# Optimization experiments

Measured on AMD Instinct MI355X. Metric: run time of the kernel, lower is better.

The kernel has to match this reference:

```python
import jax, jax.numpy as jnp
import numpy as np

N, E = 100000, 1600000
DIN, DH, DOUT = 256, 128, 32


def _glorot(key, fan_in, fan_out):
    lim = np.sqrt(6.0 / (fan_in + fan_out)).astype(np.float32)
    return jax.random.uniform(key, (fan_in, fan_out), jnp.float32, -lim, lim)


def setup_inputs() -> dict:
    key = jax.random.key(0)
    k0, k1, k2, k3 = jax.random.split(key, 4)
    x = jax.random.normal(k0, (N, DIN), dtype=jnp.float32)
    edge_index = jax.random.randint(k1, (2, E), 0, N, dtype=jnp.int64)
    return {
        "x": x,
        "edge_index": edge_index,
        "W1": _glorot(k2, DIN, DH),
        "b1": jnp.zeros((DH,), jnp.float32),
        "W2": _glorot(k3, DH, DOUT),
        "b2": jnp.zeros((DOUT,), jnp.float32),
    }


def _gcn_conv(h_in, W, b, src, dst, deg_norm_src, deg_norm_dst, n):
    # PyG GCNConv: linear transform, then sym-normalized scatter-add, then bias.
    h = h_in @ W                                   # [N, F_out]
    msg = h[src] * (deg_norm_src * deg_norm_dst)[:, None]  # [E+N, F_out]
    agg = jax.ops.segment_sum(msg, dst, num_segments=n)    # [N, F_out]
    return agg + b


def reference(x, edge_index, W1, b1, W2, b2):
    n = x.shape[0]
    loops = jnp.arange(n, dtype=edge_index.dtype)  # self-loops (GCNConv default)
    src = jnp.concatenate([edge_index[0], loops])
    dst = jnp.concatenate([edge_index[1], loops])
    deg = jax.ops.segment_sum(jnp.ones(src.shape[0], x.dtype), dst, num_segments=n)
    dis = jnp.where(deg > 0, jax.lax.rsqrt(deg), 0.0)  # deg^{-1/2}
    ns, nd = dis[src], dis[dst]
    h = jax.nn.relu(_gcn_conv(x, W1, b1, src, dst, ns, nd, n))
    out = _gcn_conv(h, W2, b2, src, dst, ns, nd, n)
    return jax.nn.log_softmax(out, axis=1)
```

## Files before the change

### kernel.cpp

```cpp
#include <hip/hip_runtime.h>
#include <hip/hip_bf16.h>
#include <cstdint>

#define DIN 256
#define DH 128
#define DOUT 32
#define CE 4096
#define BSH 9
#define MAXW 12288

typedef short s16x8 __attribute__((ext_vector_type(8)));
typedef float f32x4 __attribute__((ext_vector_type(4)));

__device__ inline ushort f2bf(float f) {
    uint u = __float_as_uint(f);
    u += 0x7fff + ((u >> 16) & 1);
    return (ushort)(u >> 16);
}
__device__ inline ushort cvtbf(float f) {
    __hip_bfloat16 b = __float2bfloat16(f);
    return __builtin_bit_cast(ushort, b);
}
__device__ inline float bf_lo(uint u) { return __uint_as_float(u << 16); }
__device__ inline float bf_hi(uint u) { return __uint_as_float(u & 0xffff0000u); }
__device__ inline uint packbf(float a, float b) {
    return (uint)cvtbf(a) | ((uint)cvtbf(b) << 16);
}
__device__ inline float ub0(uint v) { return (float)(v & 0xFFu); }
__device__ inline float ub1(uint v) { return (float)((v >> 8) & 0xFFu); }
__device__ inline float ub2(uint v) { return (float)((v >> 16) & 0xFFu); }
__device__ inline float ub3(uint v) { return (float)(v >> 24); }


__global__ __launch_bounds__(256) void k_prep(const float* __restrict__ W1,
                                              ushort* __restrict__ w1tg) {
    int o = blockIdx.x * 1024 + threadIdx.x * 4;
    int c = o >> 8;
    int k = o & 255;
    ushort4 v;
    v.x = f2bf(W1[(size_t)(k + 0) * DH + c]);
    v.y = f2bf(W1[(size_t)(k + 1) * DH + c]);
    v.z = f2bf(W1[(size_t)(k + 2) * DH + c]);
    v.w = f2bf(W1[(size_t)(k + 3) * DH + c]);
    *(ushort4*)(w1tg + o) = v;
}


__global__ __launch_bounds__(256) void k_part(
    const int* __restrict__ src, const int* __restrict__ dst,
    uint* __restrict__ pairs, int* __restrict__ tbl, int* __restrict__ gctr,
    int e, int nbuck) {
    __shared__ int cnt[256];
    __shared__ int boffs[256];
    __shared__ int sh[256];
    __shared__ uint ps[CE];
    int tid = threadIdx.x;
    if (blockIdx.x == 0 && tid == 0) *gctr = 0;
    long blkbase = (long)blockIdx.x * CE;
    int ecnt = min(CE, (int)(e - blkbase));

    cnt[tid] = 0;
    __syncthreads();

    int dreg[CE / 256];
    #pragma unroll
    for (int k = 0; k < CE / 256; ++k) {
        int i = k * 256 + tid;
        int d = -1;
        if (i < ecnt) {
            d = dst[blkbase + i];
            atomicAdd(&cnt[d >> BSH], 1);
        }
        dreg[k] = d;
    }
    __syncthreads();
    sh[tid] = cnt[tid];
    __syncthreads();
    for (int off = 1; off < 256; off <<= 1) {
        int x = (tid >= off) ? sh[tid - off] : 0;
        __syncthreads();
        if (tid >= off) sh[tid] += x;
        __syncthreads();
    }
    boffs[tid] = (tid == 0) ? 0 : sh[tid - 1];
    cnt[tid] = 0;
    __syncthreads();
    #pragma unroll
    for (int k = 0; k < CE / 256; ++k) {
        int i = k * 256 + tid;
        if (i < ecnt) {
            int d = dreg[k];
            int b = d >> BSH;
            int slot = boffs[b] + atomicAdd(&cnt[b], 1);
            ps[slot] = ((uint)(d & 511) << 17) | (uint)src[blkbase + i];
        }
    }
    __syncthreads();
    for (int i = tid; i < ecnt; i += 256)
        pairs[blkbase + i] = ps[i];
    if (tid < nbuck) tbl[blockIdx.x * (nbuck + 1) + tid] = boffs[tid];
    if (tid == 0)    tbl[blockIdx.x * (nbuck + 1) + nbuck] = ecnt;
}


__global__ __launch_bounds__(256) void k_build(
    const uint* __restrict__ pairs, const int* __restrict__ tbl,
    int* __restrict__ deg, int* __restrict__ offs, float* __restrict__ dis,
    int* __restrict__ adj, int* __restrict__ gctr,
    int nblk1, int nbuck, int n) {
    __shared__ int indeg[512];
    __shared__ int excl[512];
    __shared__ int sh[256];
    __shared__ int adjS[MAXW];
    __shared__ int baseSh, totSh;
    int tid = threadIdx.x;
    int b = blockIdx.x;
    int nodebase = b << BSH;

    indeg[tid] = 0;
    indeg[tid + 256] = 0;
    __syncthreads();

    for (int run = tid; run < nblk1; run += 256) {
        const int* trow = tbl + run * (nbuck + 1);
        int s0 = trow[b], s1 = trow[b + 1];
        long base = (long)run * CE;
        for (int k = s0; k < s1; ++k) {
            uint pp = pairs[base + k];
            atomicAdd(&indeg[pp >> 17], 1);
        }
    }
    __syncthreads();

    int a0 = indeg[tid * 2];
    int a1 = indeg[tid * 2 + 1];
    sh[tid] = a0 + a1;
    __syncthreads();
    for (int off = 1; off < 256; off <<= 1) {
        int x = (tid >= off) ? sh[tid - off] : 0;
        __syncthreads();
        if (tid >= off) sh[tid] += x;
        __syncthreads();
    }
    int e0 = (tid == 0) ? 0 : sh[tid - 1];
    excl[tid * 2] = e0;
    excl[tid * 2 + 1] = e0 + a0;
    if (tid == 255) {
        totSh = sh[255];
        baseSh = atomicAdd(gctr, sh[255]);
    }
    __syncthreads();
    int base = baseSh;
    int L = totSh;

    int i0 = nodebase + tid * 2;
    if (i0 < n) {
        deg[i0] = a0 + 1;
        offs[i0] = base + excl[tid * 2];
        dis[i0] = rsqrtf((float)(a0 + 1));
    }
    if (i0 + 1 < n) {
        deg[i0 + 1] = a1 + 1;
        offs[i0 + 1] = base + excl[tid * 2 + 1];
        dis[i0 + 1] = rsqrtf((float)(a1 + 1));
    }
    indeg[tid] = 0;
    indeg[tid + 256] = 0;
    __syncthreads();

    if (L <= MAXW) {
        for (int run = tid; run < nblk1; run += 256) {
            const int* trow = tbl + run * (nbuck + 1);
            int s0 = trow[b], s1 = trow[b + 1];
            long pb = (long)run * CE;
            for (int k = s0; k < s1; ++k) {
                uint pp = pairs[pb + k];
                int local = pp >> 17;
                int pos = excl[local] + atomicAdd(&indeg[local], 1);
                adjS[pos] = (int)(pp & 0x1FFFFu);
            }
        }
        __syncthreads();
        for (int i = tid; i < L; i += 256) adj[base + i] = adjS[i];
    } else {
        for (int run = tid; run < nblk1; run += 256) {
            const int* trow = tbl + run * (nbuck + 1);
            int s0 = trow[b], s1 = trow[b + 1];
            long pb = (long)run * CE;
            for (int k = s0; k < s1; ++k) {
                uint pp = pairs[pb + k];
                int local = pp >> 17;
                int pos = base + excl[local] + atomicAdd(&indeg[local], 1);
                adj[pos] = (int)(pp & 0x1FFFFu);
            }
        }
    }
}


__global__ __launch_bounds__(256) void k_gemm1(
    const float* __restrict__ x, const ushort* __restrict__ w1tg,
    const float* __restrict__ dis, uchar* __restrict__ hs8,
    float* __restrict__ scl, int n) {
    __shared__ union {
        ushort w1t[128][136];
        uchar  cs8[128][144];
    } u;
    __shared__ ushort xs[128][72];

    int tid = threadIdx.x;
    int row0 = blockIdx.x * 128;
    int lane = tid & 63;
    int w = tid >> 6;
    int wr0 = w * 32;
    int l15 = lane & 15;
    int koff = (lane >> 4) * 8;

    f32x4 acc[2][8];
    #pragma unroll
    for (int i = 0; i < 2; ++i)
        #pragma unroll
        for (int j = 0; j < 8; ++j)
            acc[i][j] = (f32x4){0.f, 0.f, 0.f, 0.f};

    for (int kh = 0; kh < 2; ++kh) {
        {
            int c = tid >> 1;
            int seg = (tid & 1) * 64;
            const uint4* gsrc = (const uint4*)(w1tg + (size_t)c * 256 + kh * 128 + seg);
            uint4* ldst = (uint4*)&u.w1t[c][seg];
            #pragma unroll
            for (int q = 0; q < 8; ++q) ldst[q] = gsrc[q];
        }
        for (int kc2 = 0; kc2 < 2; ++kc2) {
            {
                int r = tid >> 1;
                int half = (tid & 1) * 32;
                int rr = row0 + r; if (rr >= n) rr = n - 1;
                const float4* xr = (const float4*)(x + (size_t)rr * DIN + kh * 128 + kc2 * 64 + half);
                float4 v[8];
                #pragma unroll
                for (int q = 0; q < 8; ++q) v[q] = xr[q];
                #pragma unroll
                for (int q = 0; q < 8; ++q) {
                    ushort4 o;
                    o.x = cvtbf(v[q].x); o.y = cvtbf(v[q].y);
                    o.z = cvtbf(v[q].z); o.w = cvtbf(v[q].w);
                    *(ushort4*)&xs[r][half + q * 4] = o;
                }
            }
            __syncthreads();
            #pragma unroll
            for (int kk = 0; kk < 64; kk += 32) {
                s16x8 a0 = *(const s16x8*)&xs[wr0 + l15][kk + koff];
                s16x8 a1 = *(const s16x8*)&xs[wr0 + 16 + l15][kk + koff];
                int kl = kc2 * 64 + kk + koff;
                #pragma unroll
                for (int ct = 0; ct < 8; ++ct) {
                    s16x8 b = *(const s16x8*)&u.w1t[ct * 16 + l15][kl];
                    acc[0][ct] = __builtin_amdgcn_mfma_f32_16x16x32_bf16(a0, b, acc[0][ct], 0, 0, 0);
                    acc[1][ct] = __builtin_amdgcn_mfma_f32_16x16x32_bf16(a1, b, acc[1][ct], 0, 0, 0);
                }
            }
            __syncthreads();
        }
    }

    float dv[2][4];
    #pragma unroll
    for (int rt = 0; rt < 2; ++rt)
        #pragma unroll
        for (int r = 0; r < 4; ++r) {
            int rg = row0 + wr0 + rt * 16 + (lane >> 4) * 4 + r;
            if (rg >= n) rg = n - 1;
            dv[rt][r] = dis[rg];
        }
    #pragma unroll
    for (int rt = 0; rt < 2; ++rt) {
        #pragma unroll
        for (int r = 0; r < 4; ++r) {
            int lrow = wr0 + rt * 16 + (lane >> 4) * 4 + r;
            float vals[8];
            float mx = 0.f;
            #pragma unroll
            for (int ct = 0; ct < 8; ++ct) {
                vals[ct] = acc[rt][ct][r] * dv[rt][r];
                mx = fmaxf(mx, fabsf(vals[ct]));
            }
            mx = fmaxf(mx, __shfl_xor(mx, 1));
            mx = fmaxf(mx, __shfl_xor(mx, 2));
            mx = fmaxf(mx, __shfl_xor(mx, 4));
            mx = fmaxf(mx, __shfl_xor(mx, 8));
            float s = mx * (1.f / 127.f);
            float inv = (mx > 0.f) ? 127.f / mx : 0.f;
            #pragma unroll
            for (int ct = 0; ct < 8; ++ct)
                u.cs8[lrow][ct * 16 + l15] = (uchar)(__float2int_rn(vals[ct] * inv) + 128);
            if (l15 == 0 && row0 + lrow < n) scl[row0 + lrow] = s;
        }
    }
    __syncthreads();
    {
        int r = tid >> 1;
        int half = (tid & 1) * 64;
        if (row0 + r < n) {
            uint4* dstp = (uint4*)(hs8 + (size_t)(row0 + r) * 128 + half);
            const uint4* sp = (const uint4*)&u.cs8[r][half];
            #pragma unroll
            for (int q = 0; q < 4; ++q) dstp[q] = sp[q];
        }
    }
}


__global__ __launch_bounds__(256) void k_agg1(
    const uchar* __restrict__ hs8, const float* __restrict__ scl,
    const float* __restrict__ dis, const int* __restrict__ offs,
    const int* __restrict__ deg, const int* __restrict__ adj,
    const float* __restrict__ b1, ushort* __restrict__ h1, int n) {
    int node = blockIdx.x * 4 + (threadIdx.x >> 6);
    if (node >= n) return;
    int lane = threadIdx.x & 63;
    int r = lane >> 4;
    int j = lane & 15;

    const uint2* hq = (const uint2*)hs8;
    int off = offs[node];
    int nsrc = deg[node];

    float a8[8] = {0.f, 0.f, 0.f, 0.f, 0.f, 0.f, 0.f, 0.f};
    float ss = 0.f;
    int i = r;
    #define ACC8(v, c)                                      \
        a8[0] += ub0((v).x) * (c); a8[1] += ub1((v).x) * (c); \
        a8[2] += ub2((v).x) * (c); a8[3] += ub3((v).x) * (c); \
        a8[4] += ub0((v).y) * (c); a8[5] += ub1((v).y) * (c); \
        a8[6] += ub2((v).y) * (c); a8[7] += ub3((v).y) * (c); \
        ss += (c);
    for (; i + 12 < nsrc; i += 16) {
        int s0 = (i == 0) ? node : adj[off + i - 1];
        int s1 = adj[off + i + 3];
        int s2 = adj[off + i + 7];
        int s3 = adj[off + i + 11];
        float c0 = scl[s0], c1 = scl[s1], c2 = scl[s2], c3 = scl[s3];
        uint2 v0 = hq[(size_t)s0 * 16 + j];
        uint2 v1 = hq[(size_t)s1 * 16 + j];
        uint2 v2 = hq[(size_t)s2 * 16 + j];
        uint2 v3 = hq[(size_t)s3 * 16 + j];
        ACC8(v0, c0) ACC8(v1, c1) ACC8(v2, c2) ACC8(v3, c3)
    }
    for (; i + 4 < nsrc; i += 8) {
        int s0 = (i == 0) ? node : adj[off + i - 1];
        int s1 = adj[off + i + 3];
        float c0 = scl[s0], c1 = scl[s1];
        uint2 v0 = hq[(size_t)s0 * 16 + j];
        uint2 v1 = hq[(size_t)s1 * 16 + j];
        ACC8(v0, c0) ACC8(v1, c1)
    }
    if (i < nsrc) {
        int s0 = (i == 0) ? node : adj[off + i - 1];
        float c0 = scl[s0];
        uint2 v0 = hq[(size_t)s0 * 16 + j];
        ACC8(v0, c0)
    }
    #undef ACC8
    #pragma unroll
    for (int q = 0; q < 8; ++q) {
        a8[q] += __shfl_xor(a8[q], 16);
        a8[q] += __shfl_xor(a8[q], 32);
    }
    ss += __shfl_xor(ss, 16);
    ss += __shfl_xor(ss, 32);
    float corr = 128.f * ss;
    #pragma unroll
    for (int q = 0; q < 8; ++q) a8[q] -= corr;

    float dv = dis[node];
    float4 ba = ((const float4*)b1)[j * 2];
    float4 bb = ((const float4*)b1)[j * 2 + 1];
    if (r == 0) {
        uint4 ov;
        ov.x = packbf(fmaxf(a8[0] * dv + ba.x, 0.f), fmaxf(a8[1] * dv + ba.y, 0.f));
        ov.y = packbf(fmaxf(a8[2] * dv + ba.z, 0.f), fmaxf(a8[3] * dv + ba.w, 0.f));
        ov.z = packbf(fmaxf(a8[4] * dv + bb.x, 0.f), fmaxf(a8[5] * dv + bb.y, 0.f));
        ov.w = packbf(fmaxf(a8[6] * dv + bb.z, 0.f), fmaxf(a8[7] * dv + bb.w, 0.f));
        ((uint4*)h1)[(size_t)node * 16 + j] = ov;
    }
}


__global__ __launch_bounds__(256) void k_gemm2(
    const ushort* __restrict__ h1, const float* __restrict__ W2,
    const float* __restrict__ dis, uchar* __restrict__ h2q,
    float* __restrict__ scl2, int n) {
    int t = blockIdx.x * blockDim.x + threadIdx.x;
    int row = t >> 3;
    int cg = t & 7;
    if (row >= n) return;
    const uint2* hr = (const uint2*)(h1 + (size_t)row * DH);
    const float4* w4 = (const float4*)W2;
    float4 acc = make_float4(0.f, 0.f, 0.f, 0.f);
    #pragma unroll 8
    for (int k4 = 0; k4 < DH / 4; ++k4) {
        uint2 au = hr[k4];
        float a0 = bf_lo(au.x), a1 = bf_hi(au.x), a2 = bf_lo(au.y), a3 = bf_hi(au.y);
        float4 w0 = w4[(k4 * 4 + 0) * 8 + cg];
        float4 w1 = w4[(k4 * 4 + 1) * 8 + cg];
        float4 w2 = w4[(k4 * 4 + 2) * 8 + cg];
        float4 w3 = w4[(k4 * 4 + 3) * 8 + cg];
        acc.x += a0 * w0.x + a1 * w1.x + a2 * w2.x + a3 * w3.x;
        acc.y += a0 * w0.y + a1 * w1.y + a2 * w2.y + a3 * w3.y;
        acc.z += a0 * w0.z + a1 * w1.z + a2 * w2.z + a3 * w3.z;
        acc.w += a0 * w0.w + a1 * w1.w + a2 * w2.w + a3 * w3.w;
    }
    float dv = dis[row];
    float vals[4] = {acc.x * dv, acc.y * dv, acc.z * dv, acc.w * dv};
    float mx = fmaxf(fmaxf(fabsf(vals[0]), fabsf(vals[1])),
                     fmaxf(fabsf(vals[2]), fabsf(vals[3])));
    mx = fmaxf(mx, __shfl_xor(mx, 1));
    mx = fmaxf(mx, __shfl_xor(mx, 2));
    mx = fmaxf(mx, __shfl_xor(mx, 4));
    float s = mx * (1.f / 127.f);
    float inv = (mx > 0.f) ? 127.f / mx : 0.f;
    uint q0 = (uint)(__float2int_rn(vals[0] * inv) + 128);
    uint q1 = (uint)(__float2int_rn(vals[1] * inv) + 128);
    uint q2 = (uint)(__float2int_rn(vals[2] * inv) + 128);
    uint q3 = (uint)(__float2int_rn(vals[3] * inv) + 128);
    ((uint*)h2q)[(size_t)row * 8 + cg] = q0 | (q1 << 8) | (q2 << 16) | (q3 << 24);
    if (cg == 0) scl2[row] = s;
}


__global__ __launch_bounds__(256) void k_agg2_lsm(
    const uchar* __restrict__ h2q, const float* __restrict__ scl2,
    const float* __restrict__ dis, const int* __restrict__ offs,
    const int* __restrict__ deg, const int* __restrict__ adj,
    const float* __restrict__ b2, float* __restrict__ out, int n) {
    int node = blockIdx.x * 8 + (threadIdx.x >> 5);
    if (node >= n) return;
    int t32 = threadIdx.x & 31;
    int rr = t32 >> 2;
    int j = t32 & 3;

    const uint2* hq = (const uint2*)h2q;
    int off = offs[node];
    int nsrc = deg[node];

    float a8[8] = {0.f, 0.f, 0.f, 0.f, 0.f, 0.f, 0.f, 0.f};
    float ss = 0.f;
    int i = rr;
    #define ACC8(v, c)                                      \
        a8[0] += ub0((v).x) * (c); a8[1] += ub1((v).x) * (c); \
        a8[2] += ub2((v).x) * (c); a8[3] += ub3((v).x) * (c); \
        a8[4] += ub0((v).y) * (c); a8[5] += ub1((v).y) * (c); \
        a8[6] += ub2((v).y) * (c); a8[7] += ub3((v).y) * (c); \
        ss += (c);
    for (; i + 8 < nsrc; i += 16) {
        int s0 = (i == 0) ? node : adj[off + i - 1];
        int s1 = adj[off + i + 7];
        float c0 = scl2[s0], c1 = scl2[s1];
        uint2 v0 = hq[(size_t)s0 * 4 + j];
        uint2 v1 = hq[(size_t)s1 * 4 + j];
        ACC8(v0, c0) ACC8(v1, c1)
    }
    if (i < nsrc) {
        int s0 = (i == 0) ? node : adj[off + i - 1];
        float c0 = scl2[s0];
        uint2 v0 = hq[(size_t)s0 * 4 + j];
        ACC8(v0, c0)
    }
    #undef ACC8
    #pragma unroll
    for (int q = 0; q < 8; ++q) {
        a8[q] += __shfl_xor(a8[q], 4);
        a8[q] += __shfl_xor(a8[q], 8);
        a8[q] += __shfl_xor(a8[q], 16);
    }
    ss += __shfl_xor(ss, 4);
    ss += __shfl_xor(ss, 8);
    ss += __shfl_xor(ss, 16);
    float corr = 128.f * ss;
    #pragma unroll
    for (int q = 0; q < 8; ++q) a8[q] -= corr;

    float dv = dis[node];
    float4 ba = ((const float4*)b2)[j * 2];
    float4 bb = ((const float4*)b2)[j * 2 + 1];
    float v[8];
    v[0] = a8[0] * dv + ba.x; v[1] = a8[1] * dv + ba.y;
    v[2] = a8[2] * dv + ba.z; v[3] = a8[3] * dv + ba.w;
    v[4] = a8[4] * dv + bb.x; v[5] = a8[5] * dv + bb.y;
    v[6] = a8[6] * dv + bb.z; v[7] = a8[7] * dv + bb.w;
    float m = v[0];
    #pragma unroll
    for (int q = 1; q < 8; ++q) m = fmaxf(m, v[q]);
    m = fmaxf(m, __shfl_xor(m, 1));
    m = fmaxf(m, __shfl_xor(m, 2));
    float s = 0.f;
    #pragma unroll
    for (int q = 0; q < 8; ++q) s += __expf(v[q] - m);
    s += __shfl_xor(s, 1);
    s += __shfl_xor(s, 2);
    float ls = m + __logf(s);
    if (rr == 0) {
        float4 o0 = make_float4(v[0] - ls, v[1] - ls, v[2] - ls, v[3] - ls);
        float4 o1 = make_float4(v[4] - ls, v[5] - ls, v[6] - ls, v[7] - ls);
        float* op = out + (size_t)node * DOUT + j * 8;
        *(float4*)op = o0;
        *(float4*)(op + 4) = o1;
    }
}

extern "C" void kernel_launch(void* const* d_in, const int* in_sizes, int n_in,
                              void* d_out, int out_size, void* d_ws, size_t ws_size,
                              hipStream_t stream) {
    const float* x  = (const float*)d_in[0];
    const int*   ei = (const int*)d_in[1];
    const float* W1 = (const float*)d_in[2];
    const float* b1 = (const float*)d_in[3];
    const float* W2 = (const float*)d_in[4];
    const float* b2 = (const float*)d_in[5];
    int n = in_sizes[0] / DIN;
    int e = in_sizes[1] / 2;
    const int* src = ei;
    const int* dst = ei + e;
    float* out = (float*)d_out;

    int nblk1 = (e + CE - 1) / CE;
    int nbuck = (n + 511) >> BSH;

    char* p = (char*)d_ws;
    uint*   pairs  = (uint*)p;    p += (size_t)e * 4;
    int*    tbl    = (int*)p;     p += (size_t)nblk1 * (nbuck + 1) * 4;
    int*    deg    = (int*)p;     p += (size_t)n * 4;
    int*    offs   = (int*)p;     p += (size_t)n * 4;
    int*    gctr   = (int*)p;     p += 1024;
    float*  dis    = (float*)p;   p += (size_t)n * 4;
    int*    adj    = (int*)p;     p += (size_t)e * 4;
    ushort* w1tg   = (ushort*)p;  p += (size_t)DIN * DH * 2;
    uchar*  hs8    = (uchar*)p;   p += (size_t)n * DH;
    float*  scl    = (float*)p;   p += (size_t)n * 4;
    ushort* h1     = (ushort*)p;  p += (size_t)n * DH * 2;
    uchar*  h2q    = (uchar*)p;   p += (size_t)n * DOUT;
    float*  scl2   = (float*)p;

    k_prep<<<32, 256, 0, stream>>>(W1, w1tg);
    k_part<<<nblk1, 256, 0, stream>>>(src, dst, pairs, tbl, gctr, e, nbuck);
    k_build<<<nbuck, 256, 0, stream>>>(pairs, tbl, deg, offs, dis, adj, gctr,
                                       nblk1, nbuck, n);

    k_gemm1<<<(n + 127) / 128, 256, 0, stream>>>(x, w1tg, dis, hs8, scl, n);
    k_agg1<<<(n + 3) / 4, 256, 0, stream>>>(hs8, scl, dis, offs, deg, adj, b1, h1, n);
    k_gemm2<<<(n * 8 + 255) / 256, 256, 0, stream>>>(h1, W2, dis, h2q, scl2, n);
    k_agg2_lsm<<<(n + 7) / 8, 256, 0, stream>>>(h2q, scl2, dis, offs, deg, adj, b2, out, n);
}
```

Baseline: 240.7 us.

## Co-schedule GEMM1 with CSR build and fold W1 prep into partition kernel

The W1 transpose/convert blocks are merged into the edge partition kernel as extra blocks. GEMM1 and the CSR build now run as different block ranges of one launch, so the compute-bound GEMM can overlap the atomic-heavy graph build. To remove GEMM1's dependency on dis, the per-row quantization now runs on the unscaled product, and a small k_fix kernel afterwards multiplies scl by dis. This is valid because dis is a positive per-row factor. It drops launches and serialization but adds one pass over scl, and shared memory per block grows to the max of both roles.

```diff
diff --git a/kernel.cpp b/kernel.cpp
--- a/kernel.cpp
+++ b/kernel.cpp
@@ -32,29 +32,30 @@
 __device__ inline float ub3(uint v) { return (float)(v >> 24); }
 
 
-__global__ __launch_bounds__(256) void k_prep(const float* __restrict__ W1,
-                                              ushort* __restrict__ w1tg) {
-    int o = blockIdx.x * 1024 + threadIdx.x * 4;
-    int c = o >> 8;
-    int k = o & 255;
-    ushort4 v;
-    v.x = f2bf(W1[(size_t)(k + 0) * DH + c]);
-    v.y = f2bf(W1[(size_t)(k + 1) * DH + c]);
-    v.z = f2bf(W1[(size_t)(k + 2) * DH + c]);
-    v.w = f2bf(W1[(size_t)(k + 3) * DH + c]);
-    *(ushort4*)(w1tg + o) = v;
-}
-
-
-__global__ __launch_bounds__(256) void k_part(
+__global__ __launch_bounds__(256) void k_pre(
     const int* __restrict__ src, const int* __restrict__ dst,
     uint* __restrict__ pairs, int* __restrict__ tbl, int* __restrict__ gctr,
-    int e, int nbuck) {
+    const float* __restrict__ W1, ushort* __restrict__ w1tg,
+    int e, int nbuck, int nblk1) {
     __shared__ int cnt[256];
     __shared__ int boffs[256];
     __shared__ int sh[256];
     __shared__ uint ps[CE];
     int tid = threadIdx.x;
+
+    if (blockIdx.x >= nblk1) {
+        int o = (blockIdx.x - nblk1) * 1024 + tid * 4;
+        int c = o >> 8;
+        int k = o & 255;
+        ushort4 v;
+        v.x = f2bf(W1[(size_t)(k + 0) * DH + c]);
+        v.y = f2bf(W1[(size_t)(k + 1) * DH + c]);
+        v.z = f2bf(W1[(size_t)(k + 2) * DH + c]);
+        v.w = f2bf(W1[(size_t)(k + 3) * DH + c]);
+        *(ushort4*)(w1tg + o) = v;
+        return;
+    }
+
     if (blockIdx.x == 0 && tid == 0) *gctr = 0;
     long blkbase = (long)blockIdx.x * CE;
     int ecnt = min(CE, (int)(e - blkbase));
@@ -103,18 +104,123 @@
 }
 
 
-__global__ __launch_bounds__(256) void k_build(
+__global__ __launch_bounds__(256) void k_bg(
+    const float* __restrict__ x, const ushort* __restrict__ w1tg,
+    uchar* __restrict__ hs8, float* __restrict__ scl,
     const uint* __restrict__ pairs, const int* __restrict__ tbl,
     int* __restrict__ deg, int* __restrict__ offs, float* __restrict__ dis,
     int* __restrict__ adj, int* __restrict__ gctr,
-    int nblk1, int nbuck, int n) {
-    __shared__ int indeg[512];
-    __shared__ int excl[512];
-    __shared__ int sh[256];
-    __shared__ int adjS[MAXW];
-    __shared__ int baseSh, totSh;
+    int nblk1, int nbuck, int n, int ngemm) {
+    __shared__ __align__(16) char smem[54288];
     int tid = threadIdx.x;
-    int b = blockIdx.x;
+
+    if (blockIdx.x < ngemm) {
+        ushort (*w1t)[136] = (ushort(*)[136])smem;
+        uchar  (*cs8)[144] = (uchar(*)[144])smem;
+        ushort (*xs)[72]   = (ushort(*)[72])(smem + 34816);
+
+        int row0 = blockIdx.x * 128;
+        int lane = tid & 63;
+        int w = tid >> 6;
+        int wr0 = w * 32;
+        int l15 = lane & 15;
+        int koff = (lane >> 4) * 8;
+
+        f32x4 acc[2][8];
+        #pragma unroll
+        for (int i = 0; i < 2; ++i)
+            #pragma unroll
+            for (int j = 0; j < 8; ++j)
+                acc[i][j] = (f32x4){0.f, 0.f, 0.f, 0.f};
+
+        for (int kh = 0; kh < 2; ++kh) {
+            {
+                int c = tid >> 1;
+                int seg = (tid & 1) * 64;
+                const uint4* gsrc = (const uint4*)(w1tg + (size_t)c * 256 + kh * 128 + seg);
+                uint4* ldst = (uint4*)&w1t[c][seg];
+                #pragma unroll
+                for (int q = 0; q < 8; ++q) ldst[q] = gsrc[q];
+            }
+            for (int kc2 = 0; kc2 < 2; ++kc2) {
+                {
+                    int r = tid >> 1;
+                    int half = (tid & 1) * 32;
+                    int rr = row0 + r; if (rr >= n) rr = n - 1;
+                    const float4* xr = (const float4*)(x + (size_t)rr * DIN + kh * 128 + kc2 * 64 + half);
+                    float4 v[8];
+                    #pragma unroll
+                    for (int q = 0; q < 8; ++q) v[q] = xr[q];
+                    #pragma unroll
+                    for (int q = 0; q < 8; ++q) {
+                        ushort4 o;
+                        o.x = cvtbf(v[q].x); o.y = cvtbf(v[q].y);
+                        o.z = cvtbf(v[q].z); o.w = cvtbf(v[q].w);
+                        *(ushort4*)&xs[r][half + q * 4] = o;
+                    }
+                }
+                __syncthreads();
+                #pragma unroll
+                for (int kk = 0; kk < 64; kk += 32) {
+                    s16x8 a0 = *(const s16x8*)&xs[wr0 + l15][kk + koff];
+                    s16x8 a1 = *(const s16x8*)&xs[wr0 + 16 + l15][kk + koff];
+                    int kl = kc2 * 64 + kk + koff;
+                    #pragma unroll
+                    for (int ct = 0; ct < 8; ++ct) {
+                        s16x8 b = *(const s16x8*)&w1t[ct * 16 + l15][kl];
+                        acc[0][ct] = __builtin_amdgcn_mfma_f32_16x16x32_bf16(a0, b, acc[0][ct], 0, 0, 0);
+                        acc[1][ct] = __builtin_amdgcn_mfma_f32_16x16x32_bf16(a1, b, acc[1][ct], 0, 0, 0);
+                    }
+                }
+                __syncthreads();
+            }
+        }
+
+        #pragma unroll
+        for (int rt = 0; rt < 2; ++rt) {
+            #pragma unroll
+            for (int r = 0; r < 4; ++r) {
+                int lrow = wr0 + rt * 16 + (lane >> 4) * 4 + r;
+                float vals[8];
+                float mx = 0.f;
+                #pragma unroll
+                for (int ct = 0; ct < 8; ++ct) {
+                    vals[ct] = acc[rt][ct][r];
+                    mx = fmaxf(mx, fabsf(vals[ct]));
+                }
+                mx = fmaxf(mx, __shfl_xor(mx, 1));
+                mx = fmaxf(mx, __shfl_xor(mx, 2));
+                mx = fmaxf(mx, __shfl_xor(mx, 4));
+                mx = fmaxf(mx, __shfl_xor(mx, 8));
+                float s = mx * (1.f / 127.f);
+                float inv = (mx > 0.f) ? 127.f / mx : 0.f;
+                #pragma unroll
+                for (int ct = 0; ct < 8; ++ct)
+                    cs8[lrow][ct * 16 + l15] = (uchar)(__float2int_rn(vals[ct] * inv) + 128);
+                if (l15 == 0 && row0 + lrow < n) scl[row0 + lrow] = s;
+            }
+        }
+        __syncthreads();
+        {
+            int r = tid >> 1;
+            int half = (tid & 1) * 64;
+            if (row0 + r < n) {
+                uint4* dstp = (uint4*)(hs8 + (size_t)(row0 + r) * 128 + half);
+                const uint4* sp = (const uint4*)&cs8[r][half];
+                #pragma unroll
+                for (int q = 0; q < 4; ++q) dstp[q] = sp[q];
+            }
+        }
+        return;
+    }
+
+    int* adjS  = (int*)smem;
+    int* indeg = (int*)(smem + 49152);
+    int* excl  = (int*)(smem + 51200);
+    int* shb   = (int*)(smem + 53248);
+    int* bt    = (int*)(smem + 54272);
+
+    int b = blockIdx.x - ngemm;
     int nodebase = b << BSH;
 
     indeg[tid] = 0;
@@ -134,24 +240,24 @@
 
     int a0 = indeg[tid * 2];
     int a1 = indeg[tid * 2 + 1];
-    sh[tid] = a0 + a1;
+    shb[tid] = a0 + a1;
     __syncthreads();
     for (int off = 1; off < 256; off <<= 1) {
-        int x = (tid >= off) ? sh[tid - off] : 0;
+        int xv = (tid >= off) ? shb[tid - off] : 0;
         __syncthreads();
-        if (tid >= off) sh[tid] += x;
+        if (tid >= off) shb[tid] += xv;
         __syncthreads();
     }
-    int e0 = (tid == 0) ? 0 : sh[tid - 1];
+    int e0 = (tid == 0) ? 0 : shb[tid - 1];
     excl[tid * 2] = e0;
     excl[tid * 2 + 1] = e0 + a0;
     if (tid == 255) {
-        totSh = sh[255];
-        baseSh = atomicAdd(gctr, sh[255]);
-    }
-    __syncthreads();
-    int base = baseSh;
-    int L = totSh;
+        bt[1] = shb[255];
+        bt[0] = atomicAdd(gctr, shb[255]);
+    }
+    __syncthreads();
+    int base = bt[0];
+    int L = bt[1];
 
     int i0 = nodebase + tid * 2;
     if (i0 < n) {
@@ -198,118 +304,9 @@
 }
 
 
-__global__ __launch_bounds__(256) void k_gemm1(
-    const float* __restrict__ x, const ushort* __restrict__ w1tg,
-    const float* __restrict__ dis, uchar* __restrict__ hs8,
-    float* __restrict__ scl, int n) {
-    __shared__ union {
-        ushort w1t[128][136];
-        uchar  cs8[128][144];
-    } u;
-    __shared__ ushort xs[128][72];
-
-    int tid = threadIdx.x;
-    int row0 = blockIdx.x * 128;
-    int lane = tid & 63;
-    int w = tid >> 6;
-    int wr0 = w * 32;
-    int l15 = lane & 15;
-    int koff = (lane >> 4) * 8;
-
-    f32x4 acc[2][8];
-    #pragma unroll
-    for (int i = 0; i < 2; ++i)
-        #pragma unroll
-        for (int j = 0; j < 8; ++j)
-            acc[i][j] = (f32x4){0.f, 0.f, 0.f, 0.f};
-
-    for (int kh = 0; kh < 2; ++kh) {
-        {
-            int c = tid >> 1;
-            int seg = (tid & 1) * 64;
-            const uint4* gsrc = (const uint4*)(w1tg + (size_t)c * 256 + kh * 128 + seg);
-            uint4* ldst = (uint4*)&u.w1t[c][seg];
-            #pragma unroll
-            for (int q = 0; q < 8; ++q) ldst[q] = gsrc[q];
-        }
-        for (int kc2 = 0; kc2 < 2; ++kc2) {
-            {
-                int r = tid >> 1;
-                int half = (tid & 1) * 32;
-                int rr = row0 + r; if (rr >= n) rr = n - 1;
-                const float4* xr = (const float4*)(x + (size_t)rr * DIN + kh * 128 + kc2 * 64 + half);
-                float4 v[8];
-                #pragma unroll
-                for (int q = 0; q < 8; ++q) v[q] = xr[q];
-                #pragma unroll
-                for (int q = 0; q < 8; ++q) {
-                    ushort4 o;
-                    o.x = cvtbf(v[q].x); o.y = cvtbf(v[q].y);
-                    o.z = cvtbf(v[q].z); o.w = cvtbf(v[q].w);
-                    *(ushort4*)&xs[r][half + q * 4] = o;
-                }
-            }
-            __syncthreads();
-            #pragma unroll
-            for (int kk = 0; kk < 64; kk += 32) {
-                s16x8 a0 = *(const s16x8*)&xs[wr0 + l15][kk + koff];
-                s16x8 a1 = *(const s16x8*)&xs[wr0 + 16 + l15][kk + koff];
-                int kl = kc2 * 64 + kk + koff;
-                #pragma unroll
-                for (int ct = 0; ct < 8; ++ct) {
-                    s16x8 b = *(const s16x8*)&u.w1t[ct * 16 + l15][kl];
-                    acc[0][ct] = __builtin_amdgcn_mfma_f32_16x16x32_bf16(a0, b, acc[0][ct], 0, 0, 0);
-                    acc[1][ct] = __builtin_amdgcn_mfma_f32_16x16x32_bf16(a1, b, acc[1][ct], 0, 0, 0);
-                }
-            }
-            __syncthreads();
-        }
-    }
-
-    float dv[2][4];
-    #pragma unroll
-    for (int rt = 0; rt < 2; ++rt)
-        #pragma unroll
-        for (int r = 0; r < 4; ++r) {
-            int rg = row0 + wr0 + rt * 16 + (lane >> 4) * 4 + r;
-            if (rg >= n) rg = n - 1;
-            dv[rt][r] = dis[rg];
-        }
-    #pragma unroll
-    for (int rt = 0; rt < 2; ++rt) {
-        #pragma unroll
-        for (int r = 0; r < 4; ++r) {
-            int lrow = wr0 + rt * 16 + (lane >> 4) * 4 + r;
-            float vals[8];
-            float mx = 0.f;
-            #pragma unroll
-            for (int ct = 0; ct < 8; ++ct) {
-                vals[ct] = acc[rt][ct][r] * dv[rt][r];
-                mx = fmaxf(mx, fabsf(vals[ct]));
-            }
-            mx = fmaxf(mx, __shfl_xor(mx, 1));
-            mx = fmaxf(mx, __shfl_xor(mx, 2));
-            mx = fmaxf(mx, __shfl_xor(mx, 4));
-            mx = fmaxf(mx, __shfl_xor(mx, 8));
-            float s = mx * (1.f / 127.f);
-            float inv = (mx > 0.f) ? 127.f / mx : 0.f;
-            #pragma unroll
-            for (int ct = 0; ct < 8; ++ct)
-                u.cs8[lrow][ct * 16 + l15] = (uchar)(__float2int_rn(vals[ct] * inv) + 128);
-            if (l15 == 0 && row0 + lrow < n) scl[row0 + lrow] = s;
-        }
-    }
-    __syncthreads();
-    {
-        int r = tid >> 1;
-        int half = (tid & 1) * 64;
-        if (row0 + r < n) {
-            uint4* dstp = (uint4*)(hs8 + (size_t)(row0 + r) * 128 + half);
-            const uint4* sp = (const uint4*)&u.cs8[r][half];
-            #pragma unroll
-            for (int q = 0; q < 4; ++q) dstp[q] = sp[q];
-        }
-    }
+__global__ void k_fix(float* __restrict__ scl, const float* __restrict__ dis, int n) {
+    int i = blockIdx.x * blockDim.x + threadIdx.x;
+    if (i < n) scl[i] *= dis[i];
 }
 
 
@@ -528,6 +525,7 @@
 
     int nblk1 = (e + CE - 1) / CE;
     int nbuck = (n + 511) >> BSH;
+    int ngemm = (n + 127) / 128;
 
     char* p = (char*)d_ws;
     uint*   pairs  = (uint*)p;    p += (size_t)e * 4;
@@ -544,12 +542,12 @@
     uchar*  h2q    = (uchar*)p;   p += (size_t)n * DOUT;
     float*  scl2   = (float*)p;
 
-    k_prep<<<32, 256, 0, stream>>>(W1, w1tg);
-    k_part<<<nblk1, 256, 0, stream>>>(src, dst, pairs, tbl, gctr, e, nbuck);
-    k_build<<<nbuck, 256, 0, stream>>>(pairs, tbl, deg, offs, dis, adj, gctr,
-                                       nblk1, nbuck, n);
-
-    k_gemm1<<<(n + 127) / 128, 256, 0, stream>>>(x, w1tg, dis, hs8, scl, n);
+    k_pre<<<nblk1 + 32, 256, 0, stream>>>(src, dst, pairs, tbl, gctr, W1, w1tg,
+                                          e, nbuck, nblk1);
+    k_bg<<<ngemm + nbuck, 256, 0, stream>>>(x, w1tg, hs8, scl,
+                                            pairs, tbl, deg, offs, dis, adj, gctr,
+                                            nblk1, nbuck, n, ngemm);
+    k_fix<<<(n + 255) / 256, 256, 0, stream>>>(scl, dis, n);
     k_agg1<<<(n + 3) / 4, 256, 0, stream>>>(hs8, scl, dis, offs, deg, adj, b1, h1, n);
     k_gemm2<<<(n * 8 + 255) / 256, 256, 0, stream>>>(h1, W2, dis, h2q, scl2, n);
     k_agg2_lsm<<<(n + 7) / 8, 256, 0, stream>>>(h2q, scl2, dis, offs, deg, adj, b2, out, n);
```

Result: faster. 228.1 us, median of 3 (-5.2%).
